# Kernel optimization log

Measured on AMD Instinct MI355X. Metric: run time of the kernel, lower is better.

Reference implementation:

```python
import jax, jax.numpy as jnp
import numpy as np

B, F, E, A, T, H = 16384, 1024, 28, 2, 128, 4
HD = T // H  # head dim = 32

def _ln(x, g, b, eps=1e-5):
    m = jnp.mean(x, axis=-1, keepdims=True)
    v = jnp.var(x, axis=-1, keepdims=True)
    return (x - m) / jnp.sqrt(v + eps) * g + b

def _gelu(x):
    return jax.nn.gelu(x, approximate=False)  # torch nn.GELU default (erf)

def setup_inputs() -> dict:
    key = jax.random.key(0)
    ks = iter(jax.random.split(key, 48))
    def rn(shape, s=0.02):
        return jax.random.normal(next(ks), shape, jnp.float32) * s
    d = dict(
        fusion_feat=jax.random.normal(next(ks), (B, F), jnp.float32),
        explicit_logits=jax.random.normal(next(ks), (B, E), jnp.float32),
        implicit_logits=jax.random.normal(next(ks), (B, E), jnp.float32),
        affect_vec=jax.random.normal(next(ks), (B, A), jnp.float32),
        ln_exp_g=jnp.ones((E,), jnp.float32), ln_exp_b=jnp.zeros((E,), jnp.float32),
        W_exp=rn((E, T)), b_exp=jnp.zeros((T,), jnp.float32),
        ln_imp_g=jnp.ones((E,), jnp.float32), ln_imp_b=jnp.zeros((E,), jnp.float32),
        W_imp=rn((E, T)), b_imp=jnp.zeros((T,), jnp.float32),
        ln_aff_g=jnp.ones((A,), jnp.float32), ln_aff_b=jnp.zeros((A,), jnp.float32),
        W_aff=rn((A, T)), b_aff=jnp.zeros((T,), jnp.float32),
        Wq_in=rn((F, T)), bq_in=jnp.zeros((T,), jnp.float32),   # query_proj
        Wq=rn((T, T)), bq=jnp.zeros((T,), jnp.float32),         # MHA in_proj q
        Wk=rn((T, T)), bk=jnp.zeros((T,), jnp.float32),         # MHA in_proj k
        Wv=rn((T, T)), bv=jnp.zeros((T,), jnp.float32),         # MHA in_proj v
        Wo=rn((T, T)), bo=jnp.zeros((T,), jnp.float32),         # MHA out_proj
        Wc=rn((T, F)), bc=jnp.zeros((F,), jnp.float32),         # context_proj
        Ws=rn((3 * T, F)), bs=jnp.zeros((F,), jnp.float32),     # summary_proj
        Wg1=rn((2 * F, F)), bg1=jnp.zeros((F,), jnp.float32),   # gate layer 1
        Wg2=rn((F, F)), bg2=jnp.zeros((F,), jnp.float32),       # gate layer 2
        ln_out_g=jnp.ones((F,), jnp.float32), ln_out_b=jnp.zeros((F,), jnp.float32),
    )
    return d

def reference(fusion_feat, explicit_logits, implicit_logits, affect_vec,
              ln_exp_g, ln_exp_b, W_exp, b_exp,
              ln_imp_g, ln_imp_b, W_imp, b_imp,
              ln_aff_g, ln_aff_b, W_aff, b_aff,
              Wq_in, bq_in, Wq, bq, Wk, bk, Wv, bv, Wo, bo,
              Wc, bc, Ws, bs, Wg1, bg1, Wg2, bg2, ln_out_g, ln_out_b):
    p_exp = jax.nn.softmax(explicit_logits, axis=-1)
    p_imp = jax.nn.softmax(implicit_logits, axis=-1)
    exp_e = _gelu(_ln(p_exp, ln_exp_g, ln_exp_b) @ W_exp + b_exp)       # (B,T)
    imp_e = _gelu(_ln(p_imp, ln_imp_g, ln_imp_b) @ W_imp + b_imp)       # (B,T)
    aff_e = _gelu(_ln(affect_vec, ln_aff_g, ln_aff_b) @ W_aff + b_aff)  # (B,T)
    tokens = jnp.stack([exp_e, imp_e, aff_e], axis=1)                   # (B,3,T)
    q = fusion_feat @ Wq_in + bq_in                                     # (B,T)
    # tiny 1-query x 3-key multi-head cross attention (dropout=eval/identity)
    qh = (q @ Wq + bq).reshape(B, H, HD)
    kh = (tokens @ Wk + bk).reshape(B, 3, H, HD)
    vh = (tokens @ Wv + bv).reshape(B, 3, H, HD)
    scores = jnp.einsum('bhd,bshd->bhs', qh, kh) / np.float32(np.sqrt(HD))
    w = jax.nn.softmax(scores, axis=-1)                                 # (B,H,3)
    attn_weights = jnp.mean(w, axis=1)                                  # avg heads -> (B,3)
    attn_out = jnp.einsum('bhs,bshd->bhd', w, vh).reshape(B, T) @ Wo + bo
    context = attn_out @ Wc + bc                                        # (B,F)
    gate_h = _gelu(jnp.concatenate([fusion_feat, context], axis=-1) @ Wg1 + bg1)
    gate = jax.nn.sigmoid(gate_h @ Wg2 + bg2)
    refined = _ln(fusion_feat + gate * context, ln_out_g, ln_out_b)
    summary = _gelu(jnp.concatenate([exp_e, imp_e, aff_e], axis=-1) @ Ws + bs)
    return refined, attn_weights, summary
```

## Files before the change

kernel.cpp:

```cpp
#include <hip/hip_runtime.h>
#include <hip/hip_bf16.h>
#include <stdint.h>


using bf16 = __hip_bfloat16;
typedef __bf16 bf16x8 __attribute__((ext_vector_type(8)));
typedef float f32x4 __attribute__((ext_vector_type(4)));

__device__ __forceinline__ float b2f(bf16 x) { return __bfloat162float(x); }
__device__ __forceinline__ bf16 f2b(float x) { return __float2bfloat16(x); }

__device__ __forceinline__ float fast_tanh(float y) {
  float z = fabsf(y);
  float t = __expf(-2.f * z);
  float r = (1.f - t) / (1.f + t);
  return copysignf(r, y);
}
__device__ __forceinline__ float gelu_f(float x) {
  return 0.5f * x * (1.f + fast_tanh(0.7978845608028654f * (x + 0.044715f * x * x * x)));
}
__device__ __forceinline__ float sigmoid_f(float v) {
  return 1.f / (1.f + __expf(-v));
}

__device__ __forceinline__ void async_ld16(const void* g, void* l) {
  using GP = const __attribute__((address_space(1))) uint32_t*;
  using LP = __attribute__((address_space(3))) uint32_t*;
  __builtin_amdgcn_global_load_lds((GP)g, (LP)l, 16, 0, 0);
}

__global__ void ffb_convert(const float* __restrict__ src, bf16* __restrict__ dst) {
  size_t i = ((size_t)blockIdx.x * 256 + threadIdx.x) * 4;
  float4 v = *reinterpret_cast<const float4*>(src + i);
  ushort4 o;
  o.x = __builtin_bit_cast(unsigned short, f2b(v.x));
  o.y = __builtin_bit_cast(unsigned short, f2b(v.y));
  o.z = __builtin_bit_cast(unsigned short, f2b(v.z));
  o.w = __builtin_bit_cast(unsigned short, f2b(v.w));
  *reinterpret_cast<ushort4*>(dst + i) = o;
}

template <int EPI, typename OutT, int MT>
__launch_bounds__(256)
__global__ void gemm128(const bf16* A0, const bf16* A1, int ksplit, int lda0, int lda1,
                        const bf16* __restrict__ BT, int K,
                        const float* __restrict__ bias,
                        OutT* out, int ldo,
                        const bf16* ffp, const bf16* ctxp, int ldfc)
{
  constexpr int MIC = MT / 32;
  __shared__ uint16_t smA[MT * 64];
  __shared__ uint16_t smB[128 * 64];
  const int tid = threadIdx.x;
  const int w = tid >> 6;
  const int l = tid & 63;
  const int m0 = blockIdx.x * MT;
  const int n0 = blockIdx.y * 128;
  const int wr = w >> 1, wc = w & 1;
  const int lrow = l & 15, lquad = l >> 4;
  const int rb = w * 8 + (l >> 3);
  const int cpos = l & 7;

  const f32x4 vzero = {0.f, 0.f, 0.f, 0.f};
  f32x4 acc[MIC][4];
#pragma unroll
  for (int i = 0; i < MIC; i++)
#pragma unroll
    for (int j = 0; j < 4; j++) acc[i][j] = vzero;

  for (int k0 = 0; k0 < K; k0 += 64) {
    __syncthreads();
#pragma unroll
    for (int i = 0; i < MIC; i++) {
      int row = i * 32 + rb;
      int cg = cpos ^ (row & 7);
      int kcol = k0 + cg * 8;
      const bf16* gp = (kcol < ksplit)
                           ? (A0 + (size_t)(m0 + row) * lda0 + kcol)
                           : (A1 + (size_t)(m0 + row) * lda1 + (kcol - ksplit));
      async_ld16(gp, &smA[(i * 32 + w * 8) * 64]);
    }
#pragma unroll
    for (int i = 0; i < 4; i++) {
      int row = i * 32 + rb;
      int cg = cpos ^ (row & 7);
      const bf16* gq = BT + (size_t)(n0 + row) * K + k0 + cg * 8;
      async_ld16(gq, &smB[(i * 32 + w * 8) * 64]);
    }
    __syncthreads();
#pragma unroll
    for (int kk = 0; kk < 2; kk++) {
      bf16x8 af[MIC], bfr[4];
      const int cc = kk * 4 + lquad;
#pragma unroll
      for (int mi = 0; mi < MIC; mi++) {
        int r = wr * (MT / 2) + mi * 16 + lrow;
        af[mi] = *(const bf16x8*)&smA[r * 64 + ((cc ^ (r & 7)) << 3)];
      }
#pragma unroll
      for (int ni = 0; ni < 4; ni++) {
        int r = wc * 64 + ni * 16 + lrow;
        bfr[ni] = *(const bf16x8*)&smB[r * 64 + ((cc ^ (r & 7)) << 3)];
      }
#pragma unroll
      for (int mi = 0; mi < MIC; mi++)
#pragma unroll
        for (int ni = 0; ni < 4; ni++)
          acc[mi][ni] =
              __builtin_amdgcn_mfma_f32_16x16x32_bf16(af[mi], bfr[ni], acc[mi][ni], 0, 0, 0);
    }
  }

#pragma unroll
  for (int mi = 0; mi < MIC; mi++) {
#pragma unroll
    for (int ni = 0; ni < 4; ni++) {
#pragma unroll
      for (int r = 0; r < 4; r++) {
        int row = m0 + wr * (MT / 2) + mi * 16 + lquad * 4 + r;
        int col = n0 + wc * 64 + ni * 16 + lrow;
        float v = acc[mi][ni][r] + bias[col];
        if (EPI == 1) v = gelu_f(v);
        if (EPI == 2) {
          float gate = sigmoid_f(v);
          size_t fo = (size_t)row * ldfc + col;
          v = b2f(ffp[fo]) + gate * b2f(ctxp[fo]);
        }
        if constexpr (__is_same(OutT, float))
          out[(size_t)row * ldo + col] = v;
        else
          out[(size_t)row * ldo + col] = f2b(v);
      }
    }
  }
}

__global__ void prep_kernel(
    const float* __restrict__ Wq_in, const float* __restrict__ bq_in,
    const float* __restrict__ Wq, const float* __restrict__ bq,
    const float* __restrict__ Wk, const float* __restrict__ bk,
    const float* __restrict__ Wv, const float* __restrict__ bv,
    const float* __restrict__ Wo, const float* __restrict__ bo,
    const float* __restrict__ Wc, const float* __restrict__ bc,
    const float* __restrict__ Ws, const float* __restrict__ Wg1,
    const float* __restrict__ Wg2,
    bf16* WKVT, float* BKV, bf16* WQQT, float* BQQ, bf16* WOCT, float* BOC,
    bf16* WST, bf16* WG1T, bf16* WG2T)
{
  int idx = blockIdx.x * 256 + threadIdx.x;
  if (idx < 32768) {
    int n = idx >> 7, k = idx & 127;
    WKVT[idx] = f2b((n < 128) ? Wk[k * 128 + n] : Wv[k * 128 + (n - 128)]);
    return;
  }
  idx -= 32768;
  if (idx < 256) { BKV[idx] = (idx < 128) ? bk[idx] : bv[idx - 128]; return; }
  idx -= 256;
  if (idx < 131072) {
    int t = idx >> 10, f = idx & 1023;
    float s = 0.f;
    for (int u = 0; u < 128; u++) s += Wq_in[f * 128 + u] * Wq[u * 128 + t];
    WQQT[idx] = f2b(s);
    return;
  }
  idx -= 131072;
  if (idx < 128) {
    float s = bq[idx];
    for (int u = 0; u < 128; u++) s += bq_in[u] * Wq[u * 128 + idx];
    BQQ[idx] = s;
    return;
  }
  idx -= 128;
  if (idx < 131072) {
    int f = idx >> 7, d = idx & 127;
    float s = 0.f;
    for (int t = 0; t < 128; t++) s += Wo[d * 128 + t] * Wc[t * 1024 + f];
    WOCT[idx] = f2b(s);
    return;
  }
  idx -= 131072;
  if (idx < 1024) {
    float s = bc[idx];
    for (int t = 0; t < 128; t++) s += bo[t] * Wc[t * 1024 + idx];
    BOC[idx] = s;
    return;
  }
  idx -= 1024;
  if (idx < 393216) { int f = idx / 384, j = idx % 384; WST[idx] = f2b(Ws[j * 1024 + f]); return; }
  idx -= 393216;
  if (idx < 2097152) { int f = idx >> 11, j = idx & 2047; WG1T[idx] = f2b(Wg1[j * 1024 + f]); return; }
  idx -= 2097152;
  if (idx < 1048576) { int f = idx >> 10, j = idx & 1023; WG2T[idx] = f2b(Wg2[j * 1024 + f]); return; }
}

__device__ __forceinline__ void emb28(const float* __restrict__ logits,
                                      const float* __restrict__ g,
                                      const float* __restrict__ bb,
                                      const float* __restrict__ W,
                                      const float* __restrict__ wb,
                                      bf16* __restrict__ out, int t,
                                      float* sv, float* sp)
{
  if (t < 28) sv[t] = logits[t];
  __syncthreads();
  float mx = sv[0];
#pragma unroll
  for (int e = 1; e < 28; e++) mx = fmaxf(mx, sv[e]);
  if (t < 28) sp[t] = __expf(sv[t] - mx);
  __syncthreads();
  float sum = 0.f;
#pragma unroll
  for (int e = 0; e < 28; e++) sum += sp[e];
  float inv = 1.f / sum;
  float sp2 = 0.f;
#pragma unroll
  for (int e = 0; e < 28; e++) { float p = sp[e] * inv; sp2 += p * p; }
  const float mean = 1.f / 28.f;
  float var = sp2 * (1.f / 28.f) - mean * mean;
  float rstd = rsqrtf(var + 1e-5f);
  __syncthreads();
  if (t < 28) sp[t] = (sp[t] * inv - mean) * rstd * g[t] + bb[t];
  __syncthreads();
  float acc = wb[t];
#pragma unroll
  for (int e = 0; e < 28; e++) acc += sp[e] * W[e * 128 + t];
  out[t] = f2b(gelu_f(acc));
  __syncthreads();
}

__global__ void tokens_kernel(
    const float* __restrict__ exl, const float* __restrict__ iml, const float* __restrict__ affv,
    const float* __restrict__ geg, const float* __restrict__ geb,
    const float* __restrict__ Wex, const float* __restrict__ bex,
    const float* __restrict__ gig, const float* __restrict__ gib,
    const float* __restrict__ Wim, const float* __restrict__ bim,
    const float* __restrict__ gag, const float* __restrict__ gab,
    const float* __restrict__ Waf, const float* __restrict__ baf,
    bf16* __restrict__ tokens)
{
  __shared__ float sv[28], sp[28];
  const int b = blockIdx.x, t = threadIdx.x;
  bf16* trow = tokens + (size_t)b * 384;
  emb28(exl + (size_t)b * 28, geg, geb, Wex, bex, trow, t, sv, sp);
  emb28(iml + (size_t)b * 28, gig, gib, Wim, bim, trow + 128, t, sv, sp);
  float a0 = affv[(size_t)b * 2 + 0];
  float a1 = affv[(size_t)b * 2 + 1];
  float m = 0.5f * (a0 + a1);
  float d0 = a0 - m, d1 = a1 - m;
  float var = 0.5f * (d0 * d0 + d1 * d1);
  float rstd = rsqrtf(var + 1e-5f);
  float l0 = d0 * rstd * gag[0] + gab[0];
  float l1 = d1 * rstd * gag[1] + gab[1];
  float acc = baf[t] + l0 * Waf[t] + l1 * Waf[128 + t];
  trow[256 + t] = f2b(gelu_f(acc));
}

__global__ void attn_kernel(const bf16* __restrict__ qh, const bf16* __restrict__ kvh,
                            bf16* __restrict__ apre, float* __restrict__ attw)
{
  const int b = blockIdx.x, t = threadIdx.x;
  float q = b2f(qh[(size_t)b * 128 + t]);
  const bf16* kv = kvh + (size_t)b * 3 * 256;
  float s[3], v[3];
#pragma unroll
  for (int i = 0; i < 3; i++) {
    float k = b2f(kv[i * 256 + t]);
    v[i] = b2f(kv[i * 256 + 128 + t]);
    float r = q * k;
#pragma unroll
    for (int off = 16; off > 0; off >>= 1) r += __shfl_down(r, off, 32);
    r = __shfl(r, 0, 32);
    s[i] = r * 0.17677669529663687f;
  }
  float mx = fmaxf(s[0], fmaxf(s[1], s[2]));
  float e0 = __expf(s[0] - mx), e1 = __expf(s[1] - mx), e2 = __expf(s[2] - mx);
  float inv = 1.f / (e0 + e1 + e2);
  float w0 = e0 * inv, w1 = e1 * inv, w2 = e2 * inv;
  apre[(size_t)b * 128 + t] = f2b(w0 * v[0] + w1 * v[1] + w2 * v[2]);
  __shared__ float aw[4][3];
  if ((t & 31) == 0) { int h = t >> 5; aw[h][0] = w0; aw[h][1] = w1; aw[h][2] = w2; }
  __syncthreads();
  if (t < 3)
    attw[(size_t)b * 3 + t] = 0.25f * (aw[0][t] + aw[1][t] + aw[2][t] + aw[3][t]);
}

__global__ void ln_out_kernel(const bf16* __restrict__ x, const float* __restrict__ g,
                              const float* __restrict__ bb, float* __restrict__ out)
{
  const int row = blockIdx.x, t = threadIdx.x;
  const bf16* xr = x + (size_t)row * 1024;
  ushort4 u = *reinterpret_cast<const ushort4*>(xr + t * 4);
  float v0 = __uint_as_float((uint32_t)u.x << 16);
  float v1 = __uint_as_float((uint32_t)u.y << 16);
  float v2 = __uint_as_float((uint32_t)u.z << 16);
  float v3 = __uint_as_float((uint32_t)u.w << 16);
  float s = v0 + v1 + v2 + v3;
  float s2 = v0 * v0 + v1 * v1 + v2 * v2 + v3 * v3;
#pragma unroll
  for (int off = 32; off > 0; off >>= 1) {
    s += __shfl_down(s, off, 64);
    s2 += __shfl_down(s2, off, 64);
  }
  __shared__ float ls[4], ls2[4];
  const int w = t >> 6;
  if ((t & 63) == 0) { ls[w] = s; ls2[w] = s2; }
  __syncthreads();
  float S = ls[0] + ls[1] + ls[2] + ls[3];
  float S2 = ls2[0] + ls2[1] + ls2[2] + ls2[3];
  float mean = S * (1.f / 1024.f);
  float var = S2 * (1.f / 1024.f) - mean * mean;
  float rstd = rsqrtf(var + 1e-5f);
  const int c = t * 4;
  float4 o;
  o.x = (v0 - mean) * rstd * g[c + 0] + bb[c + 0];
  o.y = (v1 - mean) * rstd * g[c + 1] + bb[c + 1];
  o.z = (v2 - mean) * rstd * g[c + 2] + bb[c + 2];
  o.w = (v3 - mean) * rstd * g[c + 3] + bb[c + 3];
  *reinterpret_cast<float4*>(out + (size_t)row * 1024 + c) = o;
}

extern "C" void kernel_launch(void* const* d_in, const int* in_sizes, int n_in,
                              void* d_out, int out_size, void* d_ws, size_t ws_size,
                              hipStream_t stream)
{
  const float* ff   = (const float*)d_in[0];
  const float* exl  = (const float*)d_in[1];
  const float* iml  = (const float*)d_in[2];
  const float* affv = (const float*)d_in[3];
  const float* geg = (const float*)d_in[4],  *geb = (const float*)d_in[5];
  const float* Wex = (const float*)d_in[6],  *bex = (const float*)d_in[7];
  const float* gig = (const float*)d_in[8],  *gib = (const float*)d_in[9];
  const float* Wim = (const float*)d_in[10], *bim = (const float*)d_in[11];
  const float* gag = (const float*)d_in[12], *gab = (const float*)d_in[13];
  const float* Waf = (const float*)d_in[14], *baf = (const float*)d_in[15];
  const float* Wq_in = (const float*)d_in[16], *bq_in = (const float*)d_in[17];
  const float* Wq = (const float*)d_in[18], *bq = (const float*)d_in[19];
  const float* Wk = (const float*)d_in[20], *bk = (const float*)d_in[21];
  const float* Wv = (const float*)d_in[22], *bv = (const float*)d_in[23];
  const float* Wo = (const float*)d_in[24], *bo = (const float*)d_in[25];
  const float* Wc = (const float*)d_in[26], *bc = (const float*)d_in[27];
  const float* Ws = (const float*)d_in[28], *bs = (const float*)d_in[29];
  const float* Wg1 = (const float*)d_in[30], *bg1 = (const float*)d_in[31];
  const float* Wg2 = (const float*)d_in[32], *bg2 = (const float*)d_in[33];
  const float* lng = (const float*)d_in[34], *lnb = (const float*)d_in[35];

  char* ws = (char*)d_ws;
  bf16*  WKVT = (bf16*)(ws + 0);
  float* BKV  = (float*)(ws + 65536);
  bf16*  WQQT = (bf16*)(ws + 66560);
  float* BQQ  = (float*)(ws + 328704);
  bf16*  WOCT = (bf16*)(ws + 329216);
  float* BOC  = (float*)(ws + 591360);
  bf16*  WST  = (bf16*)(ws + 595456);
  bf16*  WG1T = (bf16*)(ws + 1381888);
  bf16*  WG2T = (bf16*)(ws + 5576192);
  bf16*  FFB  = (bf16*)(ws + 7673344);
  bf16*  PRE  = (bf16*)(ws + 7673344);
  bf16*  TOK  = (bf16*)(ws + 41227776);
  bf16*  QH   = (bf16*)(ws + 53810688);
  bf16*  APRE = (bf16*)(ws + 58004992);

  float* outp = (float*)d_out;
  float* out_refined = outp;
  float* out_attw    = outp + 16777216;
  float* out_summary = outp + 16826368;
  bf16* CTX   = (bf16*)out_refined;
  bf16* KVH   = (bf16*)out_summary;
  bf16* GATEH = (bf16*)out_summary;

  ffb_convert<<<16384, 256, 0, stream>>>(ff, FFB);
  prep_kernel<<<14982, 256, 0, stream>>>(Wq_in, bq_in, Wq, bq, Wk, bk, Wv, bv,
                                         Wo, bo, Wc, bc, Ws, Wg1, Wg2,
                                         WKVT, BKV, WQQT, BQQ, WOCT, BOC,
                                         WST, WG1T, WG2T);
  tokens_kernel<<<16384, 128, 0, stream>>>(exl, iml, affv, geg, geb, Wex, bex,
                                           gig, gib, Wim, bim, gag, gab, Waf, baf, TOK);
  gemm128<0, bf16, 64><<<dim3(256, 1), 256, 0, stream>>>(FFB, FFB, 1024, 1024, 1024, WQQT, 1024,
                                                         BQQ, QH, 128, nullptr, nullptr, 0);
  gemm128<0, bf16, 128><<<dim3(384, 2), 256, 0, stream>>>(TOK, TOK, 128, 128, 128, WKVT, 128,
                                                          BKV, KVH, 256, nullptr, nullptr, 0);
  attn_kernel<<<16384, 128, 0, stream>>>(QH, KVH, APRE, out_attw);
  gemm128<0, bf16, 128><<<dim3(128, 8), 256, 0, stream>>>(APRE, APRE, 128, 128, 128, WOCT, 128,
                                                          BOC, CTX, 1024, nullptr, nullptr, 0);
  gemm128<1, bf16, 128><<<dim3(128, 8), 256, 0, stream>>>(FFB, CTX, 1024, 1024, 1024, WG1T, 2048,
                                                          bg1, GATEH, 1024, nullptr, nullptr, 0);
  gemm128<2, bf16, 128><<<dim3(128, 8), 256, 0, stream>>>(GATEH, GATEH, 1024, 1024, 1024, WG2T, 1024,
                                                          bg2, PRE, 1024, FFB, CTX, 1024);
  gemm128<1, float, 128><<<dim3(128, 8), 256, 0, stream>>>(TOK, TOK, 384, 384, 384, WST, 384,
                                                           bs, out_summary, 1024, nullptr, nullptr, 0);
  ln_out_kernel<<<16384, 256, 0, stream>>>(PRE, lng, lnb, out_refined);
}
```

Baseline: 558.0 us.

## Add 256x256-tile GEMM for big layers and speed up weight prep

Adds a 512-thread gemm256 kernel with 256x256 output tiles, double-buffered async loads and setprio around the MFMAs, and uses it for the gate-1, gate-2 and summary GEMMs. Larger tiles raise operand reuse and cut L2/HBM traffic per FLOP, at the cost of fewer blocks (256) and more LDS and registers per block. Weight prep is also restructured. The naive per-element strided transposes and the O(128) scalar weight-folding loops are replaced by tiled shared-memory transposes and small MFMA GEMMs that build the fused Wq_in·Wq and Wo·Wc matrices.

```diff
diff --git a/kernel.cpp b/kernel.cpp
--- a/kernel.cpp
+++ b/kernel.cpp
@@ -119,7 +119,7 @@
       for (int r = 0; r < 4; r++) {
         int row = m0 + wr * (MT / 2) + mi * 16 + lquad * 4 + r;
         int col = n0 + wc * 64 + ni * 16 + lrow;
-        float v = acc[mi][ni][r] + bias[col];
+        float v = acc[mi][ni][r] + (bias ? bias[col] : 0.f);
         if (EPI == 1) v = gelu_f(v);
         if (EPI == 2) {
           float gate = sigmoid_f(v);
@@ -135,17 +135,161 @@
   }
 }
 
-__global__ void prep_kernel(
+template <int EPI, typename OutT>
+__launch_bounds__(512, 2)
+__global__ void gemm256(const bf16* A0, const bf16* A1, int ksplit, int lda0, int lda1,
+                        const bf16* __restrict__ BT, int K,
+                        const float* __restrict__ bias,
+                        OutT* out, int ldo,
+                        const bf16* ffp, const bf16* ctxp, int ldfc)
+{
+  __shared__ uint16_t smA[2][256 * 64];
+  __shared__ uint16_t smB[2][256 * 64];
+  const int tid = threadIdx.x;
+  const int w = tid >> 6;
+  const int l = tid & 63;
+  const int m0 = blockIdx.x * 256;
+  const int n0 = blockIdx.y * 256;
+  const int wr = w >> 2;
+  const int wc = w & 3;
+  const int lrow = l & 15, lquad = l >> 4;
+  const int rb = tid >> 3;
+  const int cpos = tid & 7;
+  const int NT = K >> 6;
+
+  const f32x4 vzero = {0.f, 0.f, 0.f, 0.f};
+  f32x4 acc[8][4];
+#pragma unroll
+  for (int mi = 0; mi < 8; mi++)
+#pragma unroll
+    for (int ni = 0; ni < 4; ni++) acc[mi][ni] = vzero;
+
+  auto stage = [&](int buf, int tt) {
+    const int k0 = tt << 6;
+    const bf16* Ab; int la, kc;
+    if (k0 < ksplit) { Ab = A0; la = lda0; kc = k0; }
+    else             { Ab = A1; la = lda1; kc = k0 - ksplit; }
+#pragma unroll
+    for (int i = 0; i < 4; i++) {
+      const int row = i * 64 + rb;
+      const int cg = cpos ^ (row & 7);
+      async_ld16(Ab + (size_t)(m0 + row) * la + kc + cg * 8,
+                 &smA[buf][(i * 64 + w * 8) * 64]);
+    }
+#pragma unroll
+    for (int i = 0; i < 4; i++) {
+      const int row = i * 64 + rb;
+      const int cg = cpos ^ (row & 7);
+      async_ld16(BT + (size_t)(n0 + row) * K + k0 + cg * 8,
+                 &smB[buf][(i * 64 + w * 8) * 64]);
+    }
+  };
+
+  int cur = 0;
+
+  auto readfrags = [&](int kk, bf16x8 (&af)[8], bf16x8 (&bfr)[4]) {
+    const int cc = kk * 4 + lquad;
+#pragma unroll
+    for (int mi = 0; mi < 8; mi++) {
+      int r = wr * 128 + mi * 16 + lrow;
+      af[mi] = *(const bf16x8*)&smA[cur][r * 64 + (((cc) ^ (r & 7)) << 3)];
+    }
+#pragma unroll
+    for (int ni = 0; ni < 4; ni++) {
+      int r = wc * 64 + ni * 16 + lrow;
+      bfr[ni] = *(const bf16x8*)&smB[cur][r * 64 + (((cc) ^ (r & 7)) << 3)];
+    }
+  };
+  auto domfma = [&](bf16x8 (&af)[8], bf16x8 (&bfr)[4]) {
+#pragma unroll
+    for (int mi = 0; mi < 8; mi++)
+#pragma unroll
+      for (int ni = 0; ni < 4; ni++)
+        acc[mi][ni] =
+            __builtin_amdgcn_mfma_f32_16x16x32_bf16(af[mi], bfr[ni], acc[mi][ni], 0, 0, 0);
+  };
+
+  stage(0, 0);
+  stage(1, 1);
+  asm volatile("s_waitcnt vmcnt(8)" ::: "memory");
+  __builtin_amdgcn_s_barrier();
+  __builtin_amdgcn_sched_barrier(0);
+
+  for (int t = 0; t < NT; ++t) {
+    bf16x8 af[8], bfr[4];
+    readfrags(0, af, bfr);
+    __builtin_amdgcn_s_setprio(1);
+    domfma(af, bfr);
+    __builtin_amdgcn_s_setprio(0);
+    readfrags(1, af, bfr);
+    asm volatile("s_waitcnt lgkmcnt(0)" ::: "memory");
+    __builtin_amdgcn_s_barrier();
+    __builtin_amdgcn_sched_barrier(0);
+    if (t + 2 < NT) stage(cur, t + 2);
+    __builtin_amdgcn_s_setprio(1);
+    domfma(af, bfr);
+    __builtin_amdgcn_s_setprio(0);
+    if (t + 2 < NT) {
+      asm volatile("s_waitcnt vmcnt(8)" ::: "memory");
+    } else {
+      asm volatile("s_waitcnt vmcnt(0)" ::: "memory");
+    }
+    __builtin_amdgcn_s_barrier();
+    __builtin_amdgcn_sched_barrier(0);
+    cur ^= 1;
+  }
+
+#pragma unroll
+  for (int mi = 0; mi < 8; mi++) {
+#pragma unroll
+    for (int ni = 0; ni < 4; ni++) {
+#pragma unroll
+      for (int r = 0; r < 4; r++) {
+        int row = m0 + wr * 128 + mi * 16 + lquad * 4 + r;
+        int col = n0 + wc * 64 + ni * 16 + lrow;
+        float v = acc[mi][ni][r] + (bias ? bias[col] : 0.f);
+        if (EPI == 1) v = gelu_f(v);
+        if (EPI == 2) {
+          float gate = sigmoid_f(v);
+          size_t fo = (size_t)row * ldfc + col;
+          v = b2f(ffp[fo]) + gate * b2f(ctxp[fo]);
+        }
+        if constexpr (__is_same(OutT, float))
+          out[(size_t)row * ldo + col] = v;
+        else
+          out[(size_t)row * ldo + col] = f2b(v);
+      }
+    }
+  }
+}
+
+__global__ void transpose_cvt(const float* __restrict__ in, bf16* __restrict__ out,
+                              int R, int C)
+{
+  __shared__ float tile[32][33];
+  const int tx = threadIdx.x & 31, ty = threadIdx.x >> 5;
+  const int c0 = blockIdx.x * 32, r0 = blockIdx.y * 32;
+#pragma unroll
+  for (int i = 0; i < 4; i++) {
+    int r = ty + i * 8;
+    tile[r][tx] = in[(size_t)(r0 + r) * C + c0 + tx];
+  }
+  __syncthreads();
+#pragma unroll
+  for (int i = 0; i < 4; i++) {
+    int c = ty + i * 8;
+    out[(size_t)(c0 + c) * R + r0 + tx] = f2b(tile[tx][c]);
+  }
+}
+
+__global__ void prep_small(
+    const float* __restrict__ Wk, const float* __restrict__ bk,
+    const float* __restrict__ Wv, const float* __restrict__ bv,
     const float* __restrict__ Wq_in, const float* __restrict__ bq_in,
     const float* __restrict__ Wq, const float* __restrict__ bq,
-    const float* __restrict__ Wk, const float* __restrict__ bk,
-    const float* __restrict__ Wv, const float* __restrict__ bv,
     const float* __restrict__ Wo, const float* __restrict__ bo,
     const float* __restrict__ Wc, const float* __restrict__ bc,
-    const float* __restrict__ Ws, const float* __restrict__ Wg1,
-    const float* __restrict__ Wg2,
-    bf16* WKVT, float* BKV, bf16* WQQT, float* BQQ, bf16* WOCT, float* BOC,
-    bf16* WST, bf16* WG1T, bf16* WG2T)
+    bf16* WKVT, float* BKV, float* BQQ, float* BOC, bf16* WQINB, bf16* WOB)
 {
   int idx = blockIdx.x * 256 + threadIdx.x;
   if (idx < 32768) {
@@ -156,14 +300,6 @@
   idx -= 32768;
   if (idx < 256) { BKV[idx] = (idx < 128) ? bk[idx] : bv[idx - 128]; return; }
   idx -= 256;
-  if (idx < 131072) {
-    int t = idx >> 10, f = idx & 1023;
-    float s = 0.f;
-    for (int u = 0; u < 128; u++) s += Wq_in[f * 128 + u] * Wq[u * 128 + t];
-    WQQT[idx] = f2b(s);
-    return;
-  }
-  idx -= 131072;
   if (idx < 128) {
     float s = bq[idx];
     for (int u = 0; u < 128; u++) s += bq_in[u] * Wq[u * 128 + idx];
@@ -171,14 +307,6 @@
     return;
   }
   idx -= 128;
-  if (idx < 131072) {
-    int f = idx >> 7, d = idx & 127;
-    float s = 0.f;
-    for (int t = 0; t < 128; t++) s += Wo[d * 128 + t] * Wc[t * 1024 + f];
-    WOCT[idx] = f2b(s);
-    return;
-  }
-  idx -= 131072;
   if (idx < 1024) {
     float s = bc[idx];
     for (int t = 0; t < 128; t++) s += bo[t] * Wc[t * 1024 + idx];
@@ -186,11 +314,9 @@
     return;
   }
   idx -= 1024;
-  if (idx < 393216) { int f = idx / 384, j = idx % 384; WST[idx] = f2b(Ws[j * 1024 + f]); return; }
-  idx -= 393216;
-  if (idx < 2097152) { int f = idx >> 11, j = idx & 2047; WG1T[idx] = f2b(Wg1[j * 1024 + f]); return; }
-  idx -= 2097152;
-  if (idx < 1048576) { int f = idx >> 10, j = idx & 1023; WG2T[idx] = f2b(Wg2[j * 1024 + f]); return; }
+  if (idx < 131072) { WQINB[idx] = f2b(Wq_in[idx]); return; }
+  idx -= 131072;
+  if (idx < 16384) { WOB[idx] = f2b(Wo[idx]); return; }
 }
 
 __device__ __forceinline__ void emb28(const float* __restrict__ logits,
@@ -360,6 +486,11 @@
   bf16*  QH   = (bf16*)(ws + 53810688);
   bf16*  APRE = (bf16*)(ws + 58004992);
 
+  bf16* WQT   = (bf16*)(ws + 53810688);
+  bf16* WOB   = (bf16*)(ws + 53810688 + 32768);
+  bf16* WQINB = (bf16*)(ws + 53810688 + 65536);
+  bf16* WCT   = (bf16*)(ws + 53810688 + 327680);
+
   float* outp = (float*)d_out;
   float* out_refined = outp;
   float* out_attw    = outp + 16777216;
@@ -369,10 +500,17 @@
   bf16* GATEH = (bf16*)out_summary;
 
   ffb_convert<<<16384, 256, 0, stream>>>(ff, FFB);
-  prep_kernel<<<14982, 256, 0, stream>>>(Wq_in, bq_in, Wq, bq, Wk, bk, Wv, bv,
-                                         Wo, bo, Wc, bc, Ws, Wg1, Wg2,
-                                         WKVT, BKV, WQQT, BQQ, WOCT, BOC,
-                                         WST, WG1T, WG2T);
+  prep_small<<<710, 256, 0, stream>>>(Wk, bk, Wv, bv, Wq_in, bq_in, Wq, bq,
+                                      Wo, bo, Wc, bc, WKVT, BKV, BQQ, BOC, WQINB, WOB);
+  transpose_cvt<<<dim3(4, 4),   256, 0, stream>>>(Wq,  WQT,  128, 128);
+  transpose_cvt<<<dim3(32, 4),  256, 0, stream>>>(Wc,  WCT,  128, 1024);
+  transpose_cvt<<<dim3(32, 12), 256, 0, stream>>>(Ws,  WST,  384, 1024);
+  transpose_cvt<<<dim3(32, 64), 256, 0, stream>>>(Wg1, WG1T, 2048, 1024);
+  transpose_cvt<<<dim3(32, 32), 256, 0, stream>>>(Wg2, WG2T, 1024, 1024);
+  gemm128<0, bf16, 128><<<dim3(1, 8), 256, 0, stream>>>(WQT, WQT, 128, 128, 128, WQINB, 128,
+                                                        nullptr, WQQT, 1024, nullptr, nullptr, 0);
+  gemm128<0, bf16, 128><<<dim3(8, 1), 256, 0, stream>>>(WCT, WCT, 128, 128, 128, WOB, 128,
+                                                        nullptr, WOCT, 128, nullptr, nullptr, 0);
   tokens_kernel<<<16384, 128, 0, stream>>>(exl, iml, affv, geg, geb, Wex, bex,
                                            gig, gib, Wim, bim, gag, gab, Waf, baf, TOK);
   gemm128<0, bf16, 64><<<dim3(256, 1), 256, 0, stream>>>(FFB, FFB, 1024, 1024, 1024, WQQT, 1024,
@@ -382,11 +520,11 @@
   attn_kernel<<<16384, 128, 0, stream>>>(QH, KVH, APRE, out_attw);
   gemm128<0, bf16, 128><<<dim3(128, 8), 256, 0, stream>>>(APRE, APRE, 128, 128, 128, WOCT, 128,
                                                           BOC, CTX, 1024, nullptr, nullptr, 0);
-  gemm128<1, bf16, 128><<<dim3(128, 8), 256, 0, stream>>>(FFB, CTX, 1024, 1024, 1024, WG1T, 2048,
-                                                          bg1, GATEH, 1024, nullptr, nullptr, 0);
-  gemm128<2, bf16, 128><<<dim3(128, 8), 256, 0, stream>>>(GATEH, GATEH, 1024, 1024, 1024, WG2T, 1024,
-                                                          bg2, PRE, 1024, FFB, CTX, 1024);
-  gemm128<1, float, 128><<<dim3(128, 8), 256, 0, stream>>>(TOK, TOK, 384, 384, 384, WST, 384,
-                                                           bs, out_summary, 1024, nullptr, nullptr, 0);
+  gemm256<1, bf16><<<dim3(64, 4), 512, 0, stream>>>(FFB, CTX, 1024, 1024, 1024, WG1T, 2048,
+                                                    bg1, GATEH, 1024, nullptr, nullptr, 0);
+  gemm256<2, bf16><<<dim3(64, 4), 512, 0, stream>>>(GATEH, GATEH, 1024, 1024, 1024, WG2T, 1024,
+                                                    bg2, PRE, 1024, FFB, CTX, 1024);
+  gemm256<1, float><<<dim3(64, 4), 512, 0, stream>>>(TOK, TOK, 384, 384, 384, WST, 384,
+                                                     bs, out_summary, 1024, nullptr, nullptr, 0);
   ln_out_kernel<<<16384, 256, 0, stream>>>(PRE, lng, lnb, out_refined);
 }
```

After: 604.7 us. 8.4% more time.
